# Optimization experiments

Measured on AMD Instinct MI355X. Metric: run time of the kernel, lower is better.

Reference implementation:

```python
import jax, jax.numpy as jnp
import numpy as np

EMBED_PHI = 1024
EMBED_F = 1024
HIDDEN_F = 1024
N_HEADS = 16
B, S = 2, 2048


def setup_inputs() -> dict:
    key = jax.random.key(0)
    ks = jax.random.split(key, 9)
    sphi = 1.0 / np.sqrt(EMBED_PHI)
    sf = 1.0 / np.sqrt(EMBED_F)
    sh = 1.0 / np.sqrt(HIDDEN_F)
    return {
        "q": jax.random.normal(ks[0], (B, S, EMBED_PHI), jnp.float32),
        "k": jax.random.normal(ks[1], (B, S, EMBED_PHI), jnp.float32),
        "v": jax.random.normal(ks[2], (B, S, EMBED_F), jnp.float32),
        "Wq": jax.random.normal(ks[3], (HIDDEN_F, EMBED_PHI), jnp.float32) * sphi,
        "Wk": jax.random.normal(ks[4], (HIDDEN_F, EMBED_PHI), jnp.float32) * sphi,
        "Wv": jax.random.normal(ks[5], (HIDDEN_F, EMBED_F), jnp.float32) * sf,
        "bv": jax.random.normal(ks[6], (HIDDEN_F,), jnp.float32) * sf,
        "Wo": jax.random.normal(ks[7], (EMBED_F, HIDDEN_F), jnp.float32) * sh,
        "bo": jax.random.normal(ks[8], (EMBED_F,), jnp.float32) * sh,
    }


def reference(q, k, v, Wq, Wk, Wv, bv, Wo, bo):
    Bq, Sq, _ = q.shape
    hd = HIDDEN_F // N_HEADS
    scale = 1.0 / np.sqrt(hd)
    # projections; torch Linear: y = x @ W.T + b
    qh = (q @ Wq.T).reshape(Bq, Sq, N_HEADS, hd).transpose(0, 2, 1, 3)  # [B,H,S,d]
    kh = (k @ Wk.T).reshape(Bq, Sq, N_HEADS, hd).transpose(0, 2, 1, 3)
    vh = (v @ Wv.T + bv).reshape(Bq, Sq, N_HEADS, hd).transpose(0, 2, 1, 3)
    scores = jnp.einsum("bhsd,bhtd->bhst", qh, kh) * scale  # [B,H,S,S]
    # mask: triu(diagonal=0) masked (attend strictly to past) except [0,0] unmasked
    mask = jnp.triu(jnp.ones((Sq, Sq), dtype=bool), k=0).at[0, 0].set(False)
    scores = jnp.where(mask, -jnp.inf, scores)
    probs = jax.nn.softmax(scores, axis=-1)  # dropout is identity at eval
    out = jnp.einsum("bhst,bhtd->bhsd", probs, vh)
    out = out.transpose(0, 2, 1, 3).reshape(Bq, Sq, HIDDEN_F)
    return out @ Wo.T + bo
```

## Files before the change

### kernel.cpp

```cpp
#include <hip/hip_runtime.h>
#include <hip/hip_bf16.h>

typedef __attribute__((ext_vector_type(8))) short short8;
typedef __attribute__((ext_vector_type(4))) float f32x4;
typedef __attribute__((ext_vector_type(4))) unsigned short us4;

#define NE  1024
#define SEQ 2048

__device__ __forceinline__ float bf2f(unsigned short u) {
    union { unsigned u; float f; } x; x.u = ((unsigned)u) << 16; return x.f;
}
__device__ __forceinline__ unsigned short f2bf(float f) {
    union { float f; unsigned u; } x; x.f = f;
    unsigned r = x.u + 0x7FFFu + ((x.u >> 16) & 1u);
    return (unsigned short)(r >> 16);
}
__device__ __forceinline__ unsigned short f2bf_fast(float f) {
    union { float f; unsigned u; } x; x.f = f;
    return (unsigned short)((x.u + 0x8000u) >> 16);
}

__global__ void detect_dtype(const unsigned short* __restrict__ s,
                             int* __restrict__ flag) {
    __shared__ int cnt;
    const int t = threadIdx.x;
    if (t == 0) cnt = 0;
    __syncthreads();
    unsigned short u = s[t];
    int e = (u >> 7) & 0xFF;
    int sane = (e == 0) || (e >= 100 && e <= 140);
    atomicAdd(&cnt, sane);
    __syncthreads();
    if (t == 0) flag[0] = (cnt >= 230) ? 1 : 0;
}

struct Ptrs7 { const void* s[7]; unsigned short* d[7]; };

__global__ void convert7(Ptrs7 p, const int* __restrict__ flag, int zoff) {
    const int z = blockIdx.z + zoff;
    const int n = (z < 3) ? (4 << 20) : (1 << 20);
    const bool in_f32 = (flag[0] == 0);
    unsigned short* d = p.d[z];
    const int stride = gridDim.x * blockDim.x;
    for (int i8 = blockIdx.x * blockDim.x + threadIdx.x; i8 * 8 < n; i8 += stride) {
        size_t off = (size_t)i8 * 8;
        if (in_f32) {
            const float* sp = (const float*)p.s[z] + off;
            float4 a = *(const float4*)sp, b2 = *(const float4*)(sp + 4);
            short8 sv;
            sv[0] = (short)f2bf(a.x);  sv[1] = (short)f2bf(a.y);
            sv[2] = (short)f2bf(a.z);  sv[3] = (short)f2bf(a.w);
            sv[4] = (short)f2bf(b2.x); sv[5] = (short)f2bf(b2.y);
            sv[6] = (short)f2bf(b2.z); sv[7] = (short)f2bf(b2.w);
            *(short8*)(d + off) = sv;
        } else {
            *(short8*)(d + off) = *(const short8*)((const unsigned short*)p.s[z] + off);
        }
    }
}

template<int AWS, int WWS, int OUTF, int VT>
__global__ __launch_bounds__(256, 3)
void gemm_bt(const void* A0, const void* A1, const void* A2,
             const void* W0, const void* W1, const void* W2,
             const void* b0, const void* b1, const void* b2,
             void* C0, void* C1, void* C2,
             const int* __restrict__ flag)
{
    __shared__ __align__(16) unsigned short As[128 * 32];
    __shared__ __align__(16) unsigned short Bs[128 * 32];
    const int z = blockIdx.z;
    const void* Ap = (z == 0) ? A0 : (z == 1) ? A1 : A2;
    const void* Wp = (z == 0) ? W0 : (z == 1) ? W1 : W2;
    const void* bp = (z == 0) ? b0 : (z == 1) ? b1 : b2;
    void*       Cp = (z == 0) ? C0 : (z == 1) ? C1 : C2;
    const bool in_f32 = (flag[0] == 0);
    const int t = threadIdx.x;
    const int w = t >> 6, l = t & 63, q = l >> 4, n = l & 15;
    const int m0 = blockIdx.y * 128, n0 = blockIdx.x * 128;
    const int wm = (w >> 1) * 64, wn = (w & 1) * 64;
    const int srow = t >> 2, sk = (t & 3) * 8;

    f32x4 acc[4][4] = {};

    for (int k0 = 0; k0 < NE; k0 += 32) {
        if (AWS || !in_f32) {
            #pragma unroll
            for (int hh = 0; hh < 2; hh++) {
                const unsigned short* ga = (const unsigned short*)Ap +
                    (size_t)(m0 + srow + hh * 64) * NE + k0 + sk;
                __builtin_amdgcn_global_load_lds(
                    (const __attribute__((address_space(1))) void*)ga,
                    (__attribute__((address_space(3))) void*)&As[hh * 2048 + w * 512],
                    16, 0, 0);
            }
        } else {
            #pragma unroll
            for (int hh = 0; hh < 2; hh++) {
                const float* a = (const float*)Ap +
                                 (size_t)(m0 + srow + hh * 64) * NE + k0 + sk;
                float4 x0 = *(const float4*)a, x1 = *(const float4*)(a + 4);
                short8 sv;
                sv[0] = (short)f2bf(x0.x); sv[1] = (short)f2bf(x0.y);
                sv[2] = (short)f2bf(x0.z); sv[3] = (short)f2bf(x0.w);
                sv[4] = (short)f2bf(x1.x); sv[5] = (short)f2bf(x1.y);
                sv[6] = (short)f2bf(x1.z); sv[7] = (short)f2bf(x1.w);
                *(short8*)(&As[hh * 2048 + t * 8]) = sv;
            }
        }
        if (WWS || !in_f32) {
            #pragma unroll
            for (int hh = 0; hh < 2; hh++) {
                const unsigned short* ga = (const unsigned short*)Wp +
                    (size_t)(n0 + srow + hh * 64) * NE + k0 + sk;
                __builtin_amdgcn_global_load_lds(
                    (const __attribute__((address_space(1))) void*)ga,
                    (__attribute__((address_space(3))) void*)&Bs[hh * 2048 + w * 512],
                    16, 0, 0);
            }
        } else {
            #pragma unroll
            for (int hh = 0; hh < 2; hh++) {
                const float* a = (const float*)Wp +
                                 (size_t)(n0 + srow + hh * 64) * NE + k0 + sk;
                float4 x0 = *(const float4*)a, x1 = *(const float4*)(a + 4);
                short8 sv;
                sv[0] = (short)f2bf(x0.x); sv[1] = (short)f2bf(x0.y);
                sv[2] = (short)f2bf(x0.z); sv[3] = (short)f2bf(x0.w);
                sv[4] = (short)f2bf(x1.x); sv[5] = (short)f2bf(x1.y);
                sv[6] = (short)f2bf(x1.z); sv[7] = (short)f2bf(x1.w);
                *(short8*)(&Bs[hh * 2048 + t * 8]) = sv;
            }
        }
        __syncthreads();

        short8 af[4], bfv[4];
        #pragma unroll
        for (int mt = 0; mt < 4; mt++)
            af[mt] = *(const short8*)(&As[(wm + mt * 16 + n) * 32 + q * 8]);
        #pragma unroll
        for (int nt = 0; nt < 4; nt++)
            bfv[nt] = *(const short8*)(&Bs[(wn + nt * 16 + n) * 32 + q * 8]);
        #pragma unroll
        for (int mt = 0; mt < 4; mt++)
            #pragma unroll
            for (int nt = 0; nt < 4; nt++)
                acc[mt][nt] = __builtin_amdgcn_mfma_f32_16x16x32_bf16(
                    af[mt], bfv[nt], acc[mt][nt], 0, 0, 0);
        __syncthreads();
    }

    #pragma unroll
    for (int mt = 0; mt < 4; mt++)
        #pragma unroll
        for (int nt = 0; nt < 4; nt++) {
            int row0 = m0 + wm + mt * 16 + q * 4;
            int col  = n0 + wn + nt * 16 + n;
            float bia = 0.f;
            if (bp)
                bia = in_f32 ? ((const float*)bp)[col]
                             : bf2f(((const unsigned short*)bp)[col]);
            if (VT && z == 2) {
                int bb = row0 >> 11, s0 = row0 & 2047;
                int hh2 = col >> 6, dd = col & 63;
                us4 pk4;
                #pragma unroll
                for (int r = 0; r < 4; r++)
                    pk4[r] = f2bf(acc[mt][nt][r] + bia);
                *(us4*)((unsigned short*)Cp +
                        ((size_t)((bb * 16 + hh2) * 64 + dd) << 11) + s0) = pk4;
            } else {
                #pragma unroll
                for (int r = 0; r < 4; r++) {
                    float v2 = acc[mt][nt][r] + bia;
                    size_t idx = (size_t)(row0 + r) * NE + col;
                    if (OUTF && in_f32) ((float*)Cp)[idx] = v2;
                    else                ((unsigned short*)Cp)[idx] = f2bf(v2);
                }
            }
        }
}

__global__ __launch_bounds__(512, 4)
void attn(const unsigned short* qh, const unsigned short* kh,
          const unsigned short* vt, unsigned short* ctx)
{
    __shared__ __align__(16) unsigned short Ks[64 * 72];
    __shared__ __align__(16) unsigned short Vt[64 * 72];
    __shared__ __align__(16) unsigned short Ps[8][16 * 72];
    const int t = threadIdx.x, w = t >> 6, l = t & 63;
    const int q = l >> 4, n = l & 15;
    const int half = w >> 2, sub = w & 3;
    const int pair = blockIdx.x;
    const int qbB = pair, qbA = 31 - pair;
    const int qb = half ? qbB : qbA;
    const int h = blockIdx.y, b = blockIdx.z;
    const size_t base = (size_t)b * SEQ * NE + h * 64;
    const size_t vbase = (size_t)((b * 16 + h) * 64) << 11;
    const int i0 = qb * 64 + sub * 16;

    short8 qf[2];
    qf[0] = *(const short8*)(&qh[base + (size_t)(i0 + n) * NE + q * 8]);
    qf[1] = *(const short8*)(&qh[base + (size_t)(i0 + n) * NE + 32 + q * 8]);

    f32x4 o[4] = {};
    float ls[4] = {0.f, 0.f, 0.f, 0.f};

    const float K1 = 0.125f * 1.4426950408889634f;
    const float B2 = 24.0f * 1.4426950408889634f;

    const int kr = t >> 3, kc = (t & 7) * 8;
    const int vd = t >> 3, vj = (t & 7) * 8;

    short8 pk, pv;
    pk = *(const short8*)(&kh[base + (size_t)kr * NE + kc]);
    pv = *(const short8*)(&vt[vbase + ((size_t)vd << 11) + vj]);

    unsigned short* PsW = &Ps[w][0];

    for (int jt = 0; jt <= qbA; jt++) {
        *(short8*)(&Ks[kr * 72 + kc]) = pk;
        *(short8*)(&Vt[vd * 72 + vj]) = pv;
        __syncthreads();

        if (jt < qbA) {
            const int jn = (jt + 1) * 64;
            pk = *(const short8*)(&kh[base + (size_t)(jn + kr) * NE + kc]);
            pv = *(const short8*)(&vt[vbase + ((size_t)vd << 11) + jn + vj]);
        }

        if (jt <= qb) {
            f32x4 sa[4] = {};
            #pragma unroll
            for (int ks = 0; ks < 2; ks++)
                #pragma unroll
                for (int nt = 0; nt < 4; nt++) {
                    short8 kf = *(const short8*)(&Ks[(nt * 16 + n) * 72 + ks * 32 + q * 8]);
                    sa[nt] = __builtin_amdgcn_mfma_f32_16x16x32_bf16(qf[ks], kf, sa[nt], 0, 0, 0);
                }

            const bool diag = (jt == qb);
            #pragma unroll
            for (int nt = 0; nt < 4; nt++)
                #pragma unroll
                for (int r = 0; r < 4; r++) {
                    float e = fmaf(sa[nt][r], K1, -B2);
                    if (diag) {
                        int j = jt * 64 + nt * 16 + n;
                        int i = i0 + q * 4 + r;
                        bool ok = (j < i) || (i == 0 && j == 0);
                        e = ok ? e : -256.0f;
                    }
                    float p = __builtin_amdgcn_exp2f(e);
                    ls[r] += p;
                    PsW[(q * 4 + r) * 72 + nt * 16 + n] = f2bf_fast(p);
                }
            asm volatile("s_waitcnt lgkmcnt(0)" ::: "memory");

            #pragma unroll
            for (int ks = 0; ks < 2; ks++) {
                short8 pf = *(const short8*)(&PsW[n * 72 + ks * 32 + q * 8]);
                #pragma unroll
                for (int dt = 0; dt < 4; dt++) {
                    short8 vf = *(const short8*)(&Vt[(dt * 16 + n) * 72 + ks * 32 + q * 8]);
                    o[dt] = __builtin_amdgcn_mfma_f32_16x16x32_bf16(pf, vf, o[dt], 0, 0, 0);
                }
            }
        }
        __syncthreads();
    }

    #pragma unroll
    for (int r = 0; r < 4; r++)
        #pragma unroll
        for (int xm = 1; xm <= 8; xm <<= 1)
            ls[r] += __shfl_xor(ls[r], xm, 64);

    #pragma unroll
    for (int r = 0; r < 4; r++) {
        float inv = 1.0f / ls[r];
        #pragma unroll
        for (int dt = 0; dt < 4; dt++)
            ctx[base + (size_t)(i0 + q * 4 + r) * NE + dt * 16 + n] =
                f2bf(o[dt][r] * inv);
    }
}

extern "C" void kernel_launch(void* const* d_in, const int* in_sizes, int n_in,
                              void* d_out, int out_size, void* d_ws, size_t ws_size,
                              hipStream_t stream) {
    const void* q  = d_in[0];
    const void* k  = d_in[1];
    const void* v  = d_in[2];
    const void* Wq = d_in[3];
    const void* Wk = d_in[4];
    const void* Wv = d_in[5];
    const void* bv = d_in[6];
    const void* Wo = d_in[7];
    const void* bo = d_in[8];

    const size_t MB = 1024 * 1024;
    const size_t M4 = 4 * MB;
    unsigned short* ws = (unsigned short*)d_ws;
    unsigned short* qh  = ws;
    unsigned short* kh  = ws + 1 * M4;
    unsigned short* vt  = ws + 2 * M4;
    unsigned short* ctx = qh;

    int tier = (ws_size >= 56 * MB + 64) ? 2 : (ws_size >= 32 * MB + 64) ? 1 : 0;

    unsigned short *qc, *kc, *vc, *Wqc, *Wkc, *Wvc, *Woc;
    int* flag;
    if (tier == 2) {
        qc = ws + 3 * M4; kc = ws + 4 * M4; vc = ws + 5 * M4;
        Wqc = ws + 6 * M4;           Wkc = Wqc + 1 * MB;
        Wvc = Wqc + 2 * MB;          Woc = Wqc + 3 * MB;
        flag = (int*)((char*)d_ws + 56 * MB);
    } else if (tier == 1) {
        qc = kc = vc = nullptr;
        Wqc = ws + 3 * M4;           Wkc = Wqc + 1 * MB;
        Wvc = Wqc + 2 * MB;          Woc = Wqc + 3 * MB;
        flag = (int*)((char*)d_ws + 32 * MB);
    } else {
        qc = kc = vc = nullptr; Wqc = Wkc = Wvc = Woc = nullptr;
        flag = (int*)((char*)d_ws + 24 * MB);
    }

    detect_dtype<<<1, 256, 0, stream>>>((const unsigned short*)q, flag);

    if (tier > 0) {
        Ptrs7 p;
        p.s[0] = q;  p.s[1] = k;  p.s[2] = v;
        p.s[3] = Wq; p.s[4] = Wk; p.s[5] = Wv; p.s[6] = Wo;
        p.d[0] = qc; p.d[1] = kc; p.d[2] = vc;
        p.d[3] = Wqc; p.d[4] = Wkc; p.d[5] = Wvc; p.d[6] = Woc;
        if (tier == 2)
            convert7<<<dim3(512, 1, 7), 256, 0, stream>>>(p, flag, 0);
        else
            convert7<<<dim3(512, 1, 4), 256, 0, stream>>>(p, flag, 3);
    }

    if (tier == 2)
        gemm_bt<1, 1, 0, 1><<<dim3(8, 32, 3), 256, 0, stream>>>(
            qc, kc, vc, Wqc, Wkc, Wvc, nullptr, nullptr, bv, qh, kh, vt, flag);
    else if (tier == 1)
        gemm_bt<0, 1, 0, 1><<<dim3(8, 32, 3), 256, 0, stream>>>(
            q, k, v, Wqc, Wkc, Wvc, nullptr, nullptr, bv, qh, kh, vt, flag);
    else
        gemm_bt<0, 0, 0, 1><<<dim3(8, 32, 3), 256, 0, stream>>>(
            q, k, v, Wq, Wk, Wv, nullptr, nullptr, bv, qh, kh, vt, flag);

    attn<<<dim3(16, 16, 2), 512, 0, stream>>>(qh, kh, vt, ctx);

    if (tier > 0)
        gemm_bt<1, 1, 1, 0><<<dim3(8, 32, 1), 256, 0, stream>>>(
            ctx, ctx, ctx, Woc, Woc, Woc, bo, bo, bo, d_out, d_out, d_out, flag);
    else
        gemm_bt<1, 0, 1, 0><<<dim3(8, 32, 1), 256, 0, stream>>>(
            ctx, ctx, ctx, Wo, Wo, Wo, bo, bo, bo, d_out, d_out, d_out, flag);
}
```

Baseline: 230.6 us.

## Double-buffer K/V tiles and transpose score MFMA for packed P writes

Double-buffers the K and V shared-memory tiles so each iteration needs one barrier instead of two, with global loads issued two tiles ahead. The score MFMA operands are swapped so each lane holds a column of scores for one query row. This allows packed bf16 conversion and 8-byte P stores to LDS, and replaces the per-row shuffle reductions with a short final reduction. It also adds s_setprio around the MFMA blocks and remaps the block order for batch 1 to spread work. Shared memory use roughly doubles for K/V, which may reduce occupancy.

```diff
diff --git a/kernel.cpp b/kernel.cpp
--- a/kernel.cpp
+++ b/kernel.cpp
@@ -4,6 +4,7 @@
 typedef __attribute__((ext_vector_type(8))) short short8;
 typedef __attribute__((ext_vector_type(4))) float f32x4;
 typedef __attribute__((ext_vector_type(4))) unsigned short us4;
+typedef __attribute__((ext_vector_type(2))) unsigned int u32x2;
 
 #define NE  1024
 #define SEQ 2048
@@ -186,16 +187,16 @@
 void attn(const unsigned short* qh, const unsigned short* kh,
           const unsigned short* vt, unsigned short* ctx)
 {
-    __shared__ __align__(16) unsigned short Ks[64 * 72];
-    __shared__ __align__(16) unsigned short Vt[64 * 72];
+    __shared__ __align__(16) unsigned short Ks[2][64 * 72];
+    __shared__ __align__(16) unsigned short Vt[2][64 * 72];
     __shared__ __align__(16) unsigned short Ps[8][16 * 72];
     const int t = threadIdx.x, w = t >> 6, l = t & 63;
     const int q = l >> 4, n = l & 15;
     const int half = w >> 2, sub = w & 3;
-    const int pair = blockIdx.x;
+    const int h = blockIdx.y, b = blockIdx.z;
+    const int pair = b ? (15 - blockIdx.x) : blockIdx.x;
     const int qbB = pair, qbA = 31 - pair;
     const int qb = half ? qbB : qbA;
-    const int h = blockIdx.y, b = blockIdx.z;
     const size_t base = (size_t)b * SEQ * NE + h * 64;
     const size_t vbase = (size_t)((b * 16 + h) * 64) << 11;
     const int i0 = qb * 64 + sub * 16;
@@ -205,7 +206,7 @@
     qf[1] = *(const short8*)(&qh[base + (size_t)(i0 + n) * NE + 32 + q * 8]);
 
     f32x4 o[4] = {};
-    float ls[4] = {0.f, 0.f, 0.f, 0.f};
+    float lsp[4] = {0.f, 0.f, 0.f, 0.f};
 
     const float K1 = 0.125f * 1.4426950408889634f;
     const float B2 = 24.0f * 1.4426950408889634f;
@@ -216,70 +217,89 @@
     short8 pk, pv;
     pk = *(const short8*)(&kh[base + (size_t)kr * NE + kc]);
     pv = *(const short8*)(&vt[vbase + ((size_t)vd << 11) + vj]);
+    *(short8*)(&Ks[0][kr * 72 + kc]) = pk;
+    *(short8*)(&Vt[0][vd * 72 + vj]) = pv;
+    if (qbA >= 1) {
+        pk = *(const short8*)(&kh[base + (size_t)(64 + kr) * NE + kc]);
+        pv = *(const short8*)(&vt[vbase + ((size_t)vd << 11) + 64 + vj]);
+    }
+    __syncthreads();
 
     unsigned short* PsW = &Ps[w][0];
+    int cur = 0;
 
     for (int jt = 0; jt <= qbA; jt++) {
-        *(short8*)(&Ks[kr * 72 + kc]) = pk;
-        *(short8*)(&Vt[vd * 72 + vj]) = pv;
-        __syncthreads();
-
-        if (jt < qbA) {
-            const int jn = (jt + 1) * 64;
+        if (jt + 1 <= qbA) {
+            *(short8*)(&Ks[cur ^ 1][kr * 72 + kc]) = pk;
+            *(short8*)(&Vt[cur ^ 1][vd * 72 + vj]) = pv;
+        }
+        if (jt + 2 <= qbA) {
+            const int jn = (jt + 2) * 64;
             pk = *(const short8*)(&kh[base + (size_t)(jn + kr) * NE + kc]);
             pv = *(const short8*)(&vt[vbase + ((size_t)vd << 11) + jn + vj]);
         }
 
         if (jt <= qb) {
+            const unsigned short* Kc = &Ks[cur][0];
+            const unsigned short* Vc = &Vt[cur][0];
             f32x4 sa[4] = {};
+            __builtin_amdgcn_s_setprio(1);
             #pragma unroll
             for (int ks = 0; ks < 2; ks++)
                 #pragma unroll
                 for (int nt = 0; nt < 4; nt++) {
-                    short8 kf = *(const short8*)(&Ks[(nt * 16 + n) * 72 + ks * 32 + q * 8]);
-                    sa[nt] = __builtin_amdgcn_mfma_f32_16x16x32_bf16(qf[ks], kf, sa[nt], 0, 0, 0);
+                    short8 kf = *(const short8*)(&Kc[(nt * 16 + n) * 72 + ks * 32 + q * 8]);
+                    sa[nt] = __builtin_amdgcn_mfma_f32_16x16x32_bf16(kf, qf[ks], sa[nt], 0, 0, 0);
                 }
+            __builtin_amdgcn_s_setprio(0);
 
             const bool diag = (jt == qb);
-            #pragma unroll
-            for (int nt = 0; nt < 4; nt++)
+            const int i = i0 + n;
+            #pragma unroll
+            for (int nt = 0; nt < 4; nt++) {
+                float p[4];
                 #pragma unroll
                 for (int r = 0; r < 4; r++) {
                     float e = fmaf(sa[nt][r], K1, -B2);
                     if (diag) {
-                        int j = jt * 64 + nt * 16 + n;
-                        int i = i0 + q * 4 + r;
+                        int j = jt * 64 + nt * 16 + q * 4 + r;
                         bool ok = (j < i) || (i == 0 && j == 0);
                         e = ok ? e : -256.0f;
                     }
-                    float p = __builtin_amdgcn_exp2f(e);
-                    ls[r] += p;
-                    PsW[(q * 4 + r) * 72 + nt * 16 + n] = f2bf_fast(p);
+                    p[r] = __builtin_amdgcn_exp2f(e);
                 }
+                lsp[nt] += (p[0] + p[1]) + (p[2] + p[3]);
+                unsigned w0, w1;
+                asm("v_cvt_pk_bf16_f32 %0, %1, %2" : "=v"(w0) : "v"(p[0]), "v"(p[1]));
+                asm("v_cvt_pk_bf16_f32 %0, %1, %2" : "=v"(w1) : "v"(p[2]), "v"(p[3]));
+                u32x2 wv; wv[0] = w0; wv[1] = w1;
+                *(u32x2*)(&PsW[n * 72 + nt * 16 + q * 4]) = wv;
+            }
             asm volatile("s_waitcnt lgkmcnt(0)" ::: "memory");
 
             #pragma unroll
             for (int ks = 0; ks < 2; ks++) {
                 short8 pf = *(const short8*)(&PsW[n * 72 + ks * 32 + q * 8]);
+                __builtin_amdgcn_s_setprio(1);
                 #pragma unroll
                 for (int dt = 0; dt < 4; dt++) {
-                    short8 vf = *(const short8*)(&Vt[(dt * 16 + n) * 72 + ks * 32 + q * 8]);
+                    short8 vf = *(const short8*)(&Vc[(dt * 16 + n) * 72 + ks * 32 + q * 8]);
                     o[dt] = __builtin_amdgcn_mfma_f32_16x16x32_bf16(pf, vf, o[dt], 0, 0, 0);
                 }
+                __builtin_amdgcn_s_setprio(0);
             }
         }
         __syncthreads();
-    }
-
-    #pragma unroll
-    for (int r = 0; r < 4; r++)
-        #pragma unroll
-        for (int xm = 1; xm <= 8; xm <<= 1)
-            ls[r] += __shfl_xor(ls[r], xm, 64);
+        cur ^= 1;
+    }
+
+    float ls = (lsp[0] + lsp[1]) + (lsp[2] + lsp[3]);
+    ls += __shfl_xor(ls, 16, 64);
+    ls += __shfl_xor(ls, 32, 64);
 
     #pragma unroll
     for (int r = 0; r < 4; r++) {
-        float inv = 1.0f / ls[r];
+        float inv = 1.0f / __shfl(ls, q * 4 + r, 64);
         #pragma unroll
         for (int dt = 0; dt < 4; dt++)
             ctx[base + (size_t)(i0 + q * 4 + r) * NE + dt * 16 + n] =
```

Measured after the change: 228.4 us. Within noise of the previous version (-0.9%).
